# Optimization experiments

Hardware: AMD Instinct MI355X
Metric: run time of the kernel (lower is better)

## Reference

```python
import jax, jax.numpy as jnp
import numpy as np

B, L, D_IN = 2, 4096, 512
H, D_K, D_V, D_OUT = 8, 64, 64, 512


def setup_inputs() -> dict:
    key = jax.random.key(0)
    k0, k1, k2, k3, k4 = jax.random.split(key, 5)
    x = jax.random.normal(k0, (B, L, D_IN), dtype=jnp.float32)
    W_q = jax.random.uniform(k1, (H, D_IN, D_K), dtype=jnp.float32)
    W_k = jax.random.uniform(k2, (H, D_IN, D_K), dtype=jnp.float32)
    W_v = jax.random.uniform(k3, (H, D_IN, D_V), dtype=jnp.float32)
    W_o = jax.random.uniform(k4, (H, D_V, D_OUT), dtype=jnp.float32)
    return {"x": x, "W_q": W_q, "W_k": W_k, "W_v": W_v, "W_o": W_o}


def reference(x, W_q, W_k, W_v, W_o):
    # x: (b, l, d_in); projections per head -> (b, h, l, d)
    Q = jnp.einsum('hjk,blj->bhlk', W_q, x)
    K = jnp.einsum('hjk,blj->bhlk', W_k, x)
    V = jnp.einsum('hjv,blj->bhlv', W_v, x)
    # no softmax: pure bilinear attention (Q K^T) V
    scores = jnp.einsum('bhik,bhjk->bhij', Q, K)          # (b, h, l, l)
    values = jnp.einsum('bhqk,bhkv->bhqv', scores, V)     # (b, h, l, d_v)
    return jnp.einsum('hvo,bhlv->blo', W_o, values)       # (b, l, d_out)
```

## Files before the change

kernel.cpp:

```cpp
#include <hip/hip_runtime.h>
#include <cstdint>


#define BDIM 2
#define LDIM 4096
#define DIN 512
#define HDIM 8
#define DK 64
#define DV 64
#define DOUT 512
#define MSPLIT 8

using bf16_t = __bf16;
typedef __bf16 bf16x8 __attribute__((ext_vector_type(8)));
typedef float floatx4 __attribute__((ext_vector_type(4)));

__device__ __forceinline__ unsigned short f2bf(float f) {
    unsigned int u = __builtin_bit_cast(unsigned int, f);
    u += 0x7FFFu + ((u >> 16) & 1u);
    return (unsigned short)(u >> 16);
}

__device__ __forceinline__ void gld_lds16(const void* g, void* l) {
    __builtin_amdgcn_global_load_lds(
        (const __attribute__((address_space(1))) void*)g,
        (__attribute__((address_space(3))) void*)l, 16, 0, 0);
}

template <int BM, int BN, int BK, bool TRANS_OUT, int OUT_MODE>
__device__ __forceinline__ void gemm_core(const bf16_t* A, const bf16_t* B,
                                          void* Cp, int K, int lda, int ldb,
                                          int ldc, int tm, int tn) {
    constexpr int WM = BM / 2, WN = BN / 2;
    constexpr int FM = WM / 16, FN = WN / 16;
    constexpr int CPR = BK / 8;
    __shared__ bf16_t As[BM * BK];
    __shared__ bf16_t Bs[BN * BK];
    const int tid = threadIdx.x;
    const int lane = tid & 63;
    const int wr = (tid >> 7) & 1;
    const int wc = (tid >> 6) & 1;

    A += (size_t)tm * lda;
    B += (size_t)tn * ldb;

    floatx4 acc[FM][FN] = {};

    for (int k0 = 0; k0 < K; k0 += BK) {
#pragma unroll
        for (int i = 0; i < (BM * CPR) / 256; ++i) {
            int c = i * 256 + tid;
            int m = c / CPR, kc = c % CPR;
            gld_lds16(A + (size_t)m * lda + k0 + kc * 8, As + c * 8);
        }
#pragma unroll
        for (int i = 0; i < (BN * CPR) / 256; ++i) {
            int c = i * 256 + tid;
            int m = c / CPR, kc = c % CPR;
            gld_lds16(B + (size_t)m * ldb + k0 + kc * 8, Bs + c * 8);
        }
        __syncthreads();

#pragma unroll
        for (int kk = 0; kk < BK; kk += 32) {
            bf16x8 aF[FM], bF[FN];
#pragma unroll
            for (int fm = 0; fm < FM; ++fm)
                aF[fm] = *(const bf16x8*)(As + (wr * WM + fm * 16 + (lane & 15)) * BK +
                                          kk + (lane >> 4) * 8);
#pragma unroll
            for (int fn = 0; fn < FN; ++fn)
                bF[fn] = *(const bf16x8*)(Bs + (wc * WN + fn * 16 + (lane & 15)) * BK +
                                          kk + (lane >> 4) * 8);
#pragma unroll
            for (int fm = 0; fm < FM; ++fm)
#pragma unroll
                for (int fn = 0; fn < FN; ++fn)
                    acc[fm][fn] = __builtin_amdgcn_mfma_f32_16x16x32_bf16(
                        aF[fm], bF[fn], acc[fm][fn], 0, 0, 0);
        }
        __syncthreads();
    }

    const int cr4 = (lane >> 4) * 4;
    const int cn = lane & 15;
#pragma unroll
    for (int fm = 0; fm < FM; ++fm)
#pragma unroll
        for (int fn = 0; fn < FN; ++fn)
#pragma unroll
            for (int r = 0; r < 4; ++r) {
                int m = tm + wr * WM + fm * 16 + cr4 + r;
                int n = tn + wc * WN + fn * 16 + cn;
                size_t idx = TRANS_OUT ? ((size_t)n * ldc + m)
                                       : ((size_t)m * ldc + n);
                if (OUT_MODE == 0)
                    ((float*)Cp)[idx] = acc[fm][fn][r];
                else if (OUT_MODE == 1)
                    ((unsigned short*)Cp)[idx] = f2bf(acc[fm][fn][r]);
                else
                    atomicAdd(&((float*)Cp)[idx], acc[fm][fn][r]);
            }
}

__global__ __launch_bounds__(256) void k_kv(const bf16_t* xb16, const bf16_t* WkvT,
                                            unsigned short* KVT) {
    int b = blockIdx.z;
    gemm_core<128, 128, 64, true, 1>(xb16 + (size_t)b * LDIM * DIN, WkvT,
                                     KVT + (size_t)b * 1024 * LDIM, DIN, DIN,
                                     DIN, LDIM, blockIdx.x * 128,
                                     blockIdx.y * 128);
}

__global__ __launch_bounds__(256) void k_msplit(const bf16_t* KVT, float* M32) {
    int s = blockIdx.x, z = blockIdx.y, b = z >> 3, h = z & 7;
    const bf16_t* base = KVT + (size_t)b * 1024 * LDIM + s * (LDIM / MSPLIT);
    const bf16_t* A = base + (size_t)(h * 64) * LDIM;
    const bf16_t* B = base + (size_t)(512 + h * 64) * LDIM;
    gemm_core<64, 64, 64, false, 2>(A, B, M32 + (size_t)z * DK * DV,
                                    LDIM / MSPLIT, LDIM, LDIM, DV, 0, 0);
}

__global__ __launch_bounds__(256) void k_tail(const bf16_t* WqC, const bf16_t* WoT,
                                              const float* M32, unsigned short* CT) {
    int i0 = blockIdx.x * 64, o0 = blockIdx.y * 64, b = blockIdx.z;
    __shared__ bf16_t Aq[64 * 64];
    __shared__ bf16_t Ws[64 * 64];
    __shared__ bf16_t Msh[64 * 64];
    __shared__ bf16_t PTs[64 * 64];
    const int tid = threadIdx.x;
    const int lane = tid & 63;
    const int wr = (tid >> 7) & 1, wc = (tid >> 6) & 1;
    const int cr4 = (lane >> 4) * 4, cn = lane & 15;

    floatx4 acc[2][2] = {};

    for (int h = 0; h < HDIM; ++h) {
#pragma unroll
        for (int i = 0; i < 2; ++i) {
            int c = i * 256 + tid, m = c >> 3, kc = c & 7;
            gld_lds16(WqC + (size_t)(i0 + m) * DIN + h * 64 + kc * 8, Aq + c * 8);
            gld_lds16(WoT + ((size_t)h * DOUT + o0 + m) * DV + kc * 8, Ws + c * 8);
        }
        const float* Mh = M32 + ((size_t)(b * HDIM + h)) * (DK * DV);
#pragma unroll
        for (int i = 0; i < 4; ++i) {
            int idx = (i * 256 + tid) * 4;
            float4 v = *(const float4*)(Mh + idx);
            *(ushort4*)((unsigned short*)Msh + idx) =
                make_ushort4(f2bf(v.x), f2bf(v.y), f2bf(v.z), f2bf(v.w));
        }
        __syncthreads();

        floatx4 pt[2][2] = {};
#pragma unroll
        for (int kk = 0; kk < 64; kk += 32) {
            bf16x8 aF[2], bF[2];
#pragma unroll
            for (int f = 0; f < 2; ++f) {
                aF[f] = *(const bf16x8*)(Ws + (wr * 32 + f * 16 + cn) * 64 + kk +
                                         (lane >> 4) * 8);
                bF[f] = *(const bf16x8*)(Msh + (wc * 32 + f * 16 + cn) * 64 + kk +
                                         (lane >> 4) * 8);
            }
#pragma unroll
            for (int fm = 0; fm < 2; ++fm)
#pragma unroll
                for (int fn = 0; fn < 2; ++fn)
                    pt[fm][fn] = __builtin_amdgcn_mfma_f32_16x16x32_bf16(
                        aF[fm], bF[fn], pt[fm][fn], 0, 0, 0);
        }
#pragma unroll
        for (int fm = 0; fm < 2; ++fm)
#pragma unroll
            for (int fn = 0; fn < 2; ++fn)
#pragma unroll
                for (int r = 0; r < 4; ++r) {
                    int m = wr * 32 + fm * 16 + cr4 + r;
                    int n = wc * 32 + fn * 16 + cn;
                    ((unsigned short*)PTs)[m * 64 + n] = f2bf(pt[fm][fn][r]);
                }
        __syncthreads();

#pragma unroll
        for (int kk = 0; kk < 64; kk += 32) {
            bf16x8 aF[2], bF[2];
#pragma unroll
            for (int f = 0; f < 2; ++f) {
                aF[f] = *(const bf16x8*)(PTs + (wr * 32 + f * 16 + cn) * 64 + kk +
                                         (lane >> 4) * 8);
                bF[f] = *(const bf16x8*)(Aq + (wc * 32 + f * 16 + cn) * 64 + kk +
                                         (lane >> 4) * 8);
            }
#pragma unroll
            for (int fm = 0; fm < 2; ++fm)
#pragma unroll
                for (int fn = 0; fn < 2; ++fn)
                    acc[fm][fn] = __builtin_amdgcn_mfma_f32_16x16x32_bf16(
                        aF[fm], bF[fn], acc[fm][fn], 0, 0, 0);
        }
        __syncthreads();
    }

    unsigned short* CTb = CT + (size_t)b * DIN * DOUT;
#pragma unroll
    for (int fm = 0; fm < 2; ++fm)
#pragma unroll
        for (int fn = 0; fn < 2; ++fn)
#pragma unroll
            for (int r = 0; r < 4; ++r) {
                int m = wr * 32 + fm * 16 + cr4 + r;
                int n = wc * 32 + fn * 16 + cn;
                CTb[(size_t)(o0 + m) * DIN + i0 + n] = f2bf(acc[fm][fn][r]);
            }
}

__global__ __launch_bounds__(256) void k_out(const bf16_t* x16, const bf16_t* CT,
                                             float* out) {
    int b = blockIdx.z;
    gemm_core<64, 128, 64, false, 0>(x16 + (size_t)b * LDIM * DIN,
                                     CT + (size_t)b * DIN * DOUT,
                                     out + (size_t)b * LDIM * DOUT, DIN, DIN,
                                     DIN, DOUT, blockIdx.x * 64,
                                     blockIdx.y * 128);
}

__global__ __launch_bounds__(256) void k_prep2(
    const float* x, const float* Wq, const float* Wk, const float* Wv,
    const float* Wo, unsigned short* xb, unsigned short* WqC,
    unsigned short* WkvT, unsigned short* WoT, float* M32) {
    __shared__ unsigned short T[64][65];
    int tr = threadIdx.x >> 4, tc4 = (threadIdx.x & 15) * 4;
    int bid = blockIdx.x;
    if (bid < 2048) {
        size_t base = ((size_t)bid * 256 + threadIdx.x) * 8;
        float4 v0 = *(const float4*)(x + base);
        float4 v1 = *(const float4*)(x + base + 4);
        unsigned short o[8] = {f2bf(v0.x), f2bf(v0.y), f2bf(v0.z), f2bf(v0.w),
                               f2bf(v1.x), f2bf(v1.y), f2bf(v1.z), f2bf(v1.w)};
        *(uint4*)(xb + base) = *(const uint4*)o;
        return;
    }
    if (bid >= 2304) {
        size_t g = ((size_t)(bid - 2304) * 256 + threadIdx.x) * 32;
        float4 z4 = make_float4(0.f, 0.f, 0.f, 0.f);
#pragma unroll
        for (int q = 0; q < 8; ++q) *(float4*)(M32 + g + q * 4) = z4;
        return;
    }
    int p_ = bid - 2048;
    int t = p_ & 7, job = (p_ >> 3) & 3, h = p_ >> 5;
    if (job == 0) {
        const float* src = Wq + (size_t)h * DIN * DK;
#pragma unroll
        for (int p = 0; p < 4; ++p) {
            int i = t * 64 + p * 16 + tr;
            float4 v = *(const float4*)(src + (size_t)i * DK + tc4);
            *(ushort4*)(WqC + (size_t)i * (HDIM * DK) + h * DK + tc4) =
                make_ushort4(f2bf(v.x), f2bf(v.y), f2bf(v.z), f2bf(v.w));
        }
        return;
    }
    const float* src;
    unsigned short* dst;
    int rows, cols, r0, c0;
    if (job == 1) {
        src = Wk + (size_t)h * DIN * DK; dst = WkvT + (size_t)(h * 64) * DIN;
        rows = DIN; cols = DK; r0 = t * 64; c0 = 0;
    } else if (job == 2) {
        src = Wv + (size_t)h * DIN * DV; dst = WkvT + (size_t)(512 + h * 64) * DIN;
        rows = DIN; cols = DV; r0 = t * 64; c0 = 0;
    } else {
        src = Wo + (size_t)h * DV * DOUT; dst = WoT + (size_t)h * DOUT * DV;
        rows = DV; cols = DOUT; r0 = 0; c0 = t * 64;
    }
#pragma unroll
    for (int p = 0; p < 4; ++p) {
        int r = p * 16 + tr;
        float4 v = *(const float4*)(src + (size_t)(r0 + r) * cols + c0 + tc4);
        T[r][tc4 + 0] = f2bf(v.x); T[r][tc4 + 1] = f2bf(v.y);
        T[r][tc4 + 2] = f2bf(v.z); T[r][tc4 + 3] = f2bf(v.w);
    }
    __syncthreads();
#pragma unroll
    for (int p = 0; p < 4; ++p) {
        int c = p * 16 + tr;
        ushort4 u = make_ushort4(T[tc4 + 0][c], T[tc4 + 1][c], T[tc4 + 2][c],
                                 T[tc4 + 3][c]);
        *(ushort4*)(dst + (size_t)(c0 + c) * rows + r0 + tc4) = u;
    }
}

extern "C" void kernel_launch(void* const* d_in, const int* in_sizes, int n_in,
                              void* d_out, int out_size, void* d_ws, size_t ws_size,
                              hipStream_t stream) {
    const float* x  = (const float*)d_in[0];
    const float* Wq = (const float*)d_in[1];
    const float* Wk = (const float*)d_in[2];
    const float* Wv = (const float*)d_in[3];
    const float* Wo = (const float*)d_in[4];
    float* out = (float*)d_out;

    unsigned short* w = (unsigned short*)d_ws;
    unsigned short* xb16  = w; w += (size_t)BDIM * LDIM * DIN;
    unsigned short* WqC   = w; w += (size_t)DIN * HDIM * DK;
    unsigned short* WkvT  = w; w += (size_t)1024 * DIN;
    unsigned short* WoT   = w; w += (size_t)HDIM * DOUT * DV;
    unsigned short* KVT   = w; w += (size_t)BDIM * 1024 * LDIM;
    unsigned short* CT    = w; w += (size_t)BDIM * DIN * DOUT;
    float* M32 = (float*)(((uintptr_t)w + 255) & ~(uintptr_t)255);

    k_prep2<<<dim3(2312), 256, 0, stream>>>(x, Wq, Wk, Wv, Wo, xb16, WqC,
                                            WkvT, WoT, M32);
    k_kv<<<dim3(32, 8, BDIM), 256, 0, stream>>>((const bf16_t*)xb16,
                                                (const bf16_t*)WkvT, KVT);
    k_msplit<<<dim3(MSPLIT, BDIM * HDIM), 256, 0, stream>>>((const bf16_t*)KVT,
                                                            M32);
    k_tail<<<dim3(8, 8, BDIM), 256, 0, stream>>>((const bf16_t*)WqC,
                                                 (const bf16_t*)WoT, M32, CT);
    k_out<<<dim3(LDIM / 64, DOUT / 128, BDIM), 256, 0, stream>>>(
        (const bf16_t*)xb16, (const bf16_t*)CT, out);
}
```

Before: 128.2 us.

## Fuse K/V projection with per-head K^T V reduction into one kernel

Replaces the separate K/V projection kernel (writing KVT to global) and split-L K^T V reduction kernel with a single kernel. Each block computes a 128-row tile of K and V for one head, stages it transposed in LDS as bf16, and computes the partial 64x64 K^T V product, which it atomically adds into M32. This removes the global round-trip of the KVT intermediate and one launch. In exchange there are many more atomic adds, with 32 tiles per head contributing, and the weight layout is interleaved per head.

```diff
diff --git a/kernel.cpp b/kernel.cpp
--- a/kernel.cpp
+++ b/kernel.cpp
@@ -9,7 +9,6 @@
 #define DK 64
 #define DV 64
 #define DOUT 512
-#define MSPLIT 8
 
 using bf16_t = __bf16;
 typedef __bf16 bf16x8 __attribute__((ext_vector_type(8)));
@@ -96,29 +95,101 @@
                                        : ((size_t)m * ldc + n);
                 if (OUT_MODE == 0)
                     ((float*)Cp)[idx] = acc[fm][fn][r];
-                else if (OUT_MODE == 1)
+                else
                     ((unsigned short*)Cp)[idx] = f2bf(acc[fm][fn][r]);
-                else
-                    atomicAdd(&((float*)Cp)[idx], acc[fm][fn][r]);
-            }
-}
-
-__global__ __launch_bounds__(256) void k_kv(const bf16_t* xb16, const bf16_t* WkvT,
-                                            unsigned short* KVT) {
-    int b = blockIdx.z;
-    gemm_core<128, 128, 64, true, 1>(xb16 + (size_t)b * LDIM * DIN, WkvT,
-                                     KVT + (size_t)b * 1024 * LDIM, DIN, DIN,
-                                     DIN, LDIM, blockIdx.x * 128,
-                                     blockIdx.y * 128);
-}
-
-__global__ __launch_bounds__(256) void k_msplit(const bf16_t* KVT, float* M32) {
-    int s = blockIdx.x, z = blockIdx.y, b = z >> 3, h = z & 7;
-    const bf16_t* base = KVT + (size_t)b * 1024 * LDIM + s * (LDIM / MSPLIT);
-    const bf16_t* A = base + (size_t)(h * 64) * LDIM;
-    const bf16_t* B = base + (size_t)(512 + h * 64) * LDIM;
-    gemm_core<64, 64, 64, false, 2>(A, B, M32 + (size_t)z * DK * DV,
-                                    LDIM / MSPLIT, LDIM, LDIM, DV, 0, 0);
+            }
+}
+
+__global__ __launch_bounds__(256) void k_kvm(const bf16_t* xb16,
+                                             const bf16_t* WkvT, float* M32) {
+    constexpr int EP = 136;
+    __shared__ bf16_t smem[128 * EP];
+    bf16_t* As = smem;
+    bf16_t* Bs = smem + 128 * 64;
+    const int lt = blockIdx.x, h = blockIdx.y, b = blockIdx.z;
+    const int tid = threadIdx.x;
+    const int lane = tid & 63;
+    const int wr = (tid >> 7) & 1, wc = (tid >> 6) & 1;
+    const int cr4 = (lane >> 4) * 4, cn = lane & 15;
+
+    const bf16_t* A = xb16 + (size_t)b * LDIM * DIN + (size_t)lt * 128 * DIN;
+    const bf16_t* B = WkvT + (size_t)h * 128 * DIN;
+
+    floatx4 acc[4][4] = {};
+    for (int k0 = 0; k0 < DIN; k0 += 64) {
+#pragma unroll
+        for (int i = 0; i < 4; ++i) {
+            int c = i * 256 + tid, m = c >> 3, kc = c & 7;
+            gld_lds16(A + (size_t)m * DIN + k0 + kc * 8, As + c * 8);
+        }
+#pragma unroll
+        for (int i = 0; i < 4; ++i) {
+            int c = i * 256 + tid, m = c >> 3, kc = c & 7;
+            gld_lds16(B + (size_t)m * DIN + k0 + kc * 8, Bs + c * 8);
+        }
+        __syncthreads();
+#pragma unroll
+        for (int kk = 0; kk < 64; kk += 32) {
+            bf16x8 aF[4], bF[4];
+#pragma unroll
+            for (int fm = 0; fm < 4; ++fm)
+                aF[fm] = *(const bf16x8*)(As + (wr * 64 + fm * 16 + cn) * 64 +
+                                          kk + (lane >> 4) * 8);
+#pragma unroll
+            for (int fn = 0; fn < 4; ++fn)
+                bF[fn] = *(const bf16x8*)(Bs + (wc * 64 + fn * 16 + cn) * 64 +
+                                          kk + (lane >> 4) * 8);
+#pragma unroll
+            for (int fm = 0; fm < 4; ++fm)
+#pragma unroll
+                for (int fn = 0; fn < 4; ++fn)
+                    acc[fm][fn] = __builtin_amdgcn_mfma_f32_16x16x32_bf16(
+                        aF[fm], bF[fn], acc[fm][fn], 0, 0, 0);
+        }
+        __syncthreads();
+    }
+
+#pragma unroll
+    for (int fm = 0; fm < 4; ++fm)
+#pragma unroll
+        for (int fn = 0; fn < 4; ++fn)
+#pragma unroll
+            for (int r = 0; r < 4; ++r) {
+                int m = wr * 64 + fm * 16 + cr4 + r;
+                int n = wc * 64 + fn * 16 + cn;
+                ((unsigned short*)smem)[n * EP + m] = f2bf(acc[fm][fn][r]);
+            }
+    __syncthreads();
+
+    floatx4 mm[2][2] = {};
+#pragma unroll
+    for (int kk = 0; kk < 128; kk += 32) {
+        bf16x8 aF[2], bF[2];
+#pragma unroll
+        for (int f = 0; f < 2; ++f) {
+            aF[f] = *(const bf16x8*)(smem + (wr * 32 + f * 16 + cn) * EP + kk +
+                                     (lane >> 4) * 8);
+            bF[f] = *(const bf16x8*)(smem + (64 + wc * 32 + f * 16 + cn) * EP +
+                                     kk + (lane >> 4) * 8);
+        }
+#pragma unroll
+        for (int fm = 0; fm < 2; ++fm)
+#pragma unroll
+            for (int fn = 0; fn < 2; ++fn)
+                mm[fm][fn] = __builtin_amdgcn_mfma_f32_16x16x32_bf16(
+                    aF[fm], bF[fn], mm[fm][fn], 0, 0, 0);
+    }
+    float* Mh = M32 + ((size_t)(b * HDIM + h)) * (DK * DV);
+#pragma unroll
+    for (int fm = 0; fm < 2; ++fm)
+#pragma unroll
+        for (int fn = 0; fn < 2; ++fn)
+#pragma unroll
+            for (int r = 0; r < 4; ++r) {
+                int dk = wr * 32 + fm * 16 + cr4 + r;
+                int v = wc * 32 + fn * 16 + cn;
+                atomicAdd(&Mh[dk * 64 + v], mm[fm][fn][r]);
+            }
 }
 
 __global__ __launch_bounds__(256) void k_tail(const bf16_t* WqC, const bf16_t* WoT,
@@ -265,13 +336,16 @@
     unsigned short* dst;
     int rows, cols, r0, c0;
     if (job == 1) {
-        src = Wk + (size_t)h * DIN * DK; dst = WkvT + (size_t)(h * 64) * DIN;
+        src = Wk + (size_t)h * DIN * DK;
+        dst = WkvT + ((size_t)h * 128) * DIN;
         rows = DIN; cols = DK; r0 = t * 64; c0 = 0;
     } else if (job == 2) {
-        src = Wv + (size_t)h * DIN * DV; dst = WkvT + (size_t)(512 + h * 64) * DIN;
+        src = Wv + (size_t)h * DIN * DV;
+        dst = WkvT + ((size_t)h * 128 + 64) * DIN;
         rows = DIN; cols = DV; r0 = t * 64; c0 = 0;
     } else {
-        src = Wo + (size_t)h * DV * DOUT; dst = WoT + (size_t)h * DOUT * DV;
+        src = Wo + (size_t)h * DV * DOUT;
+        dst = WoT + (size_t)h * DOUT * DV;
         rows = DV; cols = DOUT; r0 = 0; c0 = t * 64;
     }
 #pragma unroll
@@ -306,16 +380,13 @@
     unsigned short* WqC   = w; w += (size_t)DIN * HDIM * DK;
     unsigned short* WkvT  = w; w += (size_t)1024 * DIN;
     unsigned short* WoT   = w; w += (size_t)HDIM * DOUT * DV;
-    unsigned short* KVT   = w; w += (size_t)BDIM * 1024 * LDIM;
     unsigned short* CT    = w; w += (size_t)BDIM * DIN * DOUT;
     float* M32 = (float*)(((uintptr_t)w + 255) & ~(uintptr_t)255);
 
     k_prep2<<<dim3(2312), 256, 0, stream>>>(x, Wq, Wk, Wv, Wo, xb16, WqC,
                                             WkvT, WoT, M32);
-    k_kv<<<dim3(32, 8, BDIM), 256, 0, stream>>>((const bf16_t*)xb16,
-                                                (const bf16_t*)WkvT, KVT);
-    k_msplit<<<dim3(MSPLIT, BDIM * HDIM), 256, 0, stream>>>((const bf16_t*)KVT,
-                                                            M32);
+    k_kvm<<<dim3(LDIM / 128, HDIM, BDIM), 256, 0, stream>>>(
+        (const bf16_t*)xb16, (const bf16_t*)WkvT, M32);
     k_tail<<<dim3(8, 8, BDIM), 256, 0, stream>>>((const bf16_t*)WqC,
                                                  (const bf16_t*)WoT, M32, CT);
     k_out<<<dim3(LDIM / 64, DOUT / 128, BDIM), 256, 0, stream>>>(
```

New measurement: 123.5 us. -3.6%, faster.
